# Kernel tuning notes

Measured on AMD Instinct MI355X. Metric: run time of the kernel, lower is better.

## Reference

```python
import jax, jax.numpy as jnp
import numpy as np

M, N, C = 384, 384, 16
DN = ('NCHW', 'OIHW', 'NCHW')

def _rconv(x, w):
    # real-valued 2D cross-correlation, padding=4 (9x9 kernel, SAME)
    return jax.lax.conv_general_dilated(x, w, (1, 1), ((4, 4), (4, 4)), dimension_numbers=DN)

def _cconv(x, w):
    # complex conv2d decomposed into 4 real convs (matches torch complex conv2d)
    xr, xi, wr, wi = x.real, x.imag, w.real, w.imag
    return (_rconv(xr, wr) - _rconv(xi, wi)) + 1j * (_rconv(xr, wi) + _rconv(xi, wr))

def setup_inputs() -> dict:
    key = jax.random.key(0)
    ks = jax.random.split(key, 8)
    shp = (1, M, N, 2 * C)
    kspace = jax.random.normal(ks[0], shp, jnp.float32)
    row_keep = (jax.random.uniform(ks[1], (M,)) < 0.45).astype(jnp.float32)
    kspace = kspace * row_keep[None, :, None, None]
    z = 0.1 * jax.random.normal(ks[2], shp, jnp.float32)
    prev_kspace = 0.1 * jax.random.normal(ks[3], shp, jnp.float32)
    kernel_r = 0.05 * jax.random.normal(ks[4], (1, 81, C, C), jnp.float32)
    kernel_i = 0.05 * jax.random.normal(ks[5], (1, 81, C, C), jnp.float32)
    miu = jnp.array([0.05], jnp.float32)
    spirit_kernels = jnp.zeros((1,), jnp.float32)  # unused by the module's math
    return {"z": z, "kspace": kspace, "kernel_r": kernel_r, "kernel_i": kernel_i,
            "spirit_kernels": spirit_kernels, "prev_kspace": prev_kspace, "miu": miu}

def _forward(z, kspace, kernel_r, kernel_i, prev_kspace, miu):
    divp = kspace.shape[3] // 2
    kk = kspace[0, :, :, :divp] + 1j * kspace[0, :, :, divp:]  # [m,n,C] complex64
    m, n, no_c = kk.shape
    locs = jnp.abs(kk) > 0                                     # sampling mask
    K = (kernel_r[0] + 1j * kernel_i[0]).reshape(9, 9, no_c, no_c)
    # forward SPIRiT weight: Wf[co,ci,p,q] = K[q,p,ci,co]  (torch permute (3,2,1,0))
    Wf = jnp.transpose(K, (3, 2, 1, 0))
    # adjoint weight: conj, spatial flip, swap in/out channels (exact conv_backward_new)
    Wb = jnp.transpose(jnp.conj(jnp.flip(Wf, (2, 3))), (1, 0, 2, 3))

    def G(x, W):  # [m,n,C] -> [m,n,C] via NCHW complex conv
        y = _cconv(jnp.transpose(x, (2, 0, 1))[None], W)
        return jnp.transpose(y[0], (1, 2, 0))

    mask = lambda x: jnp.where(locs, x, 0)  # selection_operator followed by its adjoint

    def ATA(x):  # x: [1,m,n,C]
        x0 = x[0]
        a2 = mask(x0)                # D^T D x
        b1 = G(x0, Wf) - x0          # (G - I) x
        b2 = G(b1, Wb) - b1          # (G - I)^H (G - I) x
        return (a2 + b2)[None]       # rho = 1

    ws = prev_kspace[:, :, :, :divp] + 1j * prev_kspace[:, :, :, divp:]
    zc = z[:, :, :, :divp] + 1j * z[:, :, :, divp:]
    am = jnp.abs(miu[0])
    DTy = mask(kk)[None]             # D^T D y (y = sampled k-space)
    p = DTy + am * zc - ATA(ws) - am * ws
    r = p
    b = ws

    def step(carry, _):
        b, p, r = carry
        q = ATA(p) + am * p
        rr = jnp.sum(r * jnp.conj(r))
        alpha = rr / jnp.sum(q * jnp.conj(p))
        b_n = b + alpha * p
        r_n = r - alpha * q
        p_n = r_n + (jnp.sum(r_n * jnp.conj(r_n)) / rr) * p
        return (b_n, p_n, r_n), None

    (b, _, _), _ = jax.lax.scan(step, (b, p, r), None, length=10)
    return jnp.concatenate([jnp.real(b), jnp.imag(b)], axis=3)

def reference(z, kspace, kernel_r, kernel_i, spirit_kernels, prev_kspace, miu):
    return _forward(z, kspace, kernel_r, kernel_i, prev_kspace, miu)
```

## Files before the change

kernel.cpp:

```cpp
#include <hip/hip_runtime.h>
#include <stdint.h>


#define MM 384
#define NPIX (MM*MM)
#define N2 (16*NPIX)
#define NRED 512
#define NCBLK 768

typedef __attribute__((ext_vector_type(8))) short short8;
typedef __attribute__((ext_vector_type(4))) float f32x4;
typedef unsigned int u32;

__device__ __forceinline__ float2 block_reduce2(float2 v) {
    #pragma unroll
    for (int off = 32; off > 0; off >>= 1) {
        v.x += __shfl_down(v.x, off);
        v.y += __shfl_down(v.y, off);
    }
    __shared__ float2 tmp[8];
    const int wid = threadIdx.x >> 6, lid = threadIdx.x & 63;
    if (lid == 0) tmp[wid] = v;
    __syncthreads();
    if (threadIdx.x == 0) {
        const int nw = blockDim.x >> 6;
        for (int i = 1; i < nw; ++i) { v.x += tmp[i].x; v.y += tmp[i].y; }
    }
    return v;
}

__device__ __forceinline__ u32 bf16rn(float f) {
    const u32 u = __float_as_uint(f);
    return (u + 0x7FFFu + ((u >> 16) & 1u)) >> 16;
}

__global__ void prep_weights(const float* __restrict__ kr, const float* __restrict__ ki,
                             u32* __restrict__ wbuf) {
    const int e = blockIdx.x * 256 + threadIdx.x;
    if (e >= 20736) return;
    const int lane = e & 63;
    int r = e >> 6;
    const int hf = r & 1; r >>= 1;
    const int q = r % 9; r /= 9;
    const int p = r % 9; r /= 9;
    const int dir = r;
    const int co = lane & 15, g = lane >> 4;
    float vv[8];
    #pragma unroll
    for (int t = 0; t < 8; ++t) {
        const int kc = 8 * g + t;
        const int ci = kc & 15;
        const int isI = kc >> 4;
        int sidx;
        if (dir == 0) sidx = (q*9 + p)*256 + ci*16 + co;
        else          sidx = ((8-q)*9 + (8-p))*256 + co*16 + ci;
        const float wr = kr[sidx];
        const float wi = (dir == 0) ? ki[sidx] : -ki[sidx];
        vv[t] = (hf == 0) ? (isI ? -wi : wr) : (isI ? wr : wi);
    }
    u32 pk[4];
    #pragma unroll
    for (int t = 0; t < 4; ++t) pk[t] = bf16rn(vv[2*t]) | (bf16rn(vv[2*t+1]) << 16);
    u32* o = wbuf + (size_t)(dir*162 + (q*9 + p)*2 + hf)*256 + lane*4;
    *(uint4*)o = make_uint4(pk[0], pk[1], pk[2], pk[3]);
}

__global__ void prep_fields(const float* __restrict__ ks, const float* __restrict__ prev,
                            float2* __restrict__ wsf, uint8_t* __restrict__ mask8) {
    const int pix = blockIdx.x * blockDim.x + threadIdx.x;
    if (pix >= NPIX) return;
    #pragma unroll
    for (int c = 0; c < 16; ++c) {
        const float krr = ks[(size_t)pix*32 + c];
        const float kii = ks[(size_t)pix*32 + c + 16];
        mask8[(size_t)c*NPIX + pix] = (krr != 0.f || kii != 0.f) ? 1 : 0;
        wsf[(size_t)c*NPIX + pix] = make_float2(prev[(size_t)pix*32 + c], prev[(size_t)pix*32 + c + 16]);
    }
}

template<int MODE>
__global__ __launch_bounds__(384, 5)
void conv9(const float2* __restrict__ x, const u32* __restrict__ Wd,
           float2* __restrict__ out, float2* __restrict__ out2,
           const float2* __restrict__ aux, const float* __restrict__ ks,
           const float* __restrict__ z, const uint8_t* __restrict__ mask8,
           const float* __restrict__ miu, float2* __restrict__ partials)
{
    __shared__ __align__(16) char Xs[20*24*64];
    __shared__ __align__(16) char Wsh[9*2048];
    const int t = threadIdx.x;
    const int bi0 = blockIdx.x;
    const int bi = (bi0 & 7) * 96 + (bi0 >> 3);
    const int i0 = (bi / 24) * 12;
    const int j0 = (bi % 24) * 16;
    const int w = t >> 6, lane = t & 63;
    const int hf = (w >= 3) ? 1 : 0;
    const int wr = w - 3*hf;
    const int m = lane & 15, g = lane >> 4;

    for (int u = t; u < 20*24; u += 384) {
        const int col = u % 24, row = u / 24;
        const int row_g = i0 - 4 + row, col_g = j0 - 4 + col;
        const bool valid = ((unsigned)row_g < MM) && ((unsigned)col_g < MM);
        const float2* src = x + (size_t)row_g*MM + col_g;
        float2 v[16];
        #pragma unroll
        for (int ci = 0; ci < 16; ++ci)
            v[ci] = valid ? src[(size_t)ci*NPIX] : make_float2(0.f, 0.f);
        u32 c0[4], c1[4], c2[4], c3[4];
        #pragma unroll
        for (int j = 0; j < 4; ++j) {
            c0[j] = bf16rn(v[2*j].x)     | (bf16rn(v[2*j+1].x) << 16);
            c1[j] = bf16rn(v[8+2*j].x)   | (bf16rn(v[9+2*j].x) << 16);
            c2[j] = bf16rn(v[2*j].y)     | (bf16rn(v[2*j+1].y) << 16);
            c3[j] = bf16rn(v[8+2*j].y)   | (bf16rn(v[9+2*j].y) << 16);
        }
        const int k3 = col & 3;
        char* pb = Xs + (size_t)(row*24 + col)*64;
        *(uint4*)(pb + (((0 ^ k3)) << 4)) = make_uint4(c0[0], c0[1], c0[2], c0[3]);
        *(uint4*)(pb + (((1 ^ k3)) << 4)) = make_uint4(c1[0], c1[1], c1[2], c1[3]);
        *(uint4*)(pb + (((2 ^ k3)) << 4)) = make_uint4(c2[0], c2[1], c2[2], c2[3]);
        *(uint4*)(pb + (((3 ^ k3)) << 4)) = make_uint4(c3[0], c3[1], c3[2], c3[3]);
    }
    __syncthreads();

    f32x4 acc[4];
    #pragma unroll
    for (int a = 0; a < 4; ++a) acc[a] = (f32x4){0.f, 0.f, 0.f, 0.f};

    const char* WdC = (const char*)Wd;
    const char* wls = Wsh + (hf << 10) + (lane << 4);

    #define MFQ(Xa, Xb, Xc, Xd, WS) do { \
        acc[0] = __builtin_amdgcn_mfma_f32_16x16x32_bf16(WS, Xa, acc[0], 0, 0, 0); \
        acc[1] = __builtin_amdgcn_mfma_f32_16x16x32_bf16(WS, Xb, acc[1], 0, 0, 0); \
        acc[2] = __builtin_amdgcn_mfma_f32_16x16x32_bf16(WS, Xc, acc[2], 0, 0, 0); \
        acc[3] = __builtin_amdgcn_mfma_f32_16x16x32_bf16(WS, Xd, acc[3], 0, 0, 0); } while (0)

    #pragma unroll 1
    for (int qq = 0; qq < 9; ++qq) {
        if (qq) __syncthreads();
        {
            const uint4* wsrc = (const uint4*)(WdC + (size_t)qq * 18432);
            uint4* wdst = (uint4*)Wsh;
            wdst[t]       = wsrc[t];
            wdst[t + 384] = wsrc[t + 384];
            wdst[t + 768] = wsrc[t + 768];
        }
        __syncthreads();

        const int colq = m + qq;
        const char* xb = Xs + (size_t)((4*wr)*24 + colq)*64 + ((g ^ (colq & 3)) << 4);
        short8 X0 = *(const short8*)(xb);
        short8 X1 = *(const short8*)(xb + 1536);
        short8 X2 = *(const short8*)(xb + 2*1536);
        short8 X3 = *(const short8*)(xb + 3*1536);
        short8 X4, WT;
        WT = *(const short8*)(wls);          X4 = *(const short8*)(xb + 4*1536);  MFQ(X0, X1, X2, X3, WT);
        WT = *(const short8*)(wls + 2048);   X0 = *(const short8*)(xb + 5*1536);  MFQ(X1, X2, X3, X4, WT);
        WT = *(const short8*)(wls + 4096);   X1 = *(const short8*)(xb + 6*1536);  MFQ(X2, X3, X4, X0, WT);
        WT = *(const short8*)(wls + 6144);   X2 = *(const short8*)(xb + 7*1536);  MFQ(X3, X4, X0, X1, WT);
        WT = *(const short8*)(wls + 8192);   X3 = *(const short8*)(xb + 8*1536);  MFQ(X4, X0, X1, X2, WT);
        WT = *(const short8*)(wls + 10240);  X4 = *(const short8*)(xb + 9*1536);  MFQ(X0, X1, X2, X3, WT);
        WT = *(const short8*)(wls + 12288);  X0 = *(const short8*)(xb + 10*1536); MFQ(X1, X2, X3, X4, WT);
        WT = *(const short8*)(wls + 14336);  X1 = *(const short8*)(xb + 11*1536); MFQ(X2, X3, X4, X0, WT);
        WT = *(const short8*)(wls + 16384);                                       MFQ(X3, X4, X0, X1, WT);
    }
    #undef MFQ

    __syncthreads();
    {
        char* base = Xs + (size_t)(((hf*12 + 4*wr)*16) + m)*64 + ((g ^ (m & 3)) << 4);
        *(f32x4*)(base)        = acc[0];
        *(f32x4*)(base + 1024) = acc[1];
        *(f32x4*)(base + 2048) = acc[2];
        *(f32x4*)(base + 3072) = acc[3];
    }
    __syncthreads();

    const float am = (MODE >= 1) ? fabsf(miu[0]) : 0.f;
    float2 part = make_float2(0.f, 0.f);
    {
        const int pair = t >> 1, ch = t & 1;
        const int co = pair & 15, row = pair >> 4;
        const int gs = co >> 2, js = co & 3;
        float re[8], im[8];
        #pragma unroll
        for (int k = 0; k < 8; ++k) {
            const int col = ch*8 + k;
            const int off = (row*16 + col)*64 + ((gs ^ (col & 3)) << 4) + js*4;
            re[k] = *(const float*)(Xs + off);
            im[k] = *(const float*)(Xs + off + 12288);
        }
        const int pixb = (i0 + row)*MM + j0 + ch*8;
        const size_t gidx = (size_t)co*NPIX + pixb;
        #pragma unroll
        for (int k = 0; k < 8; ++k) {
            if (MODE == 0) {
                const float2 tc = x[gidx + k];
                out[gidx + k] = make_float2(re[k] - tc.x, im[k] - tc.y);
            } else if (MODE == 1) {
                const float2 tc = x[gidx + k];
                const float2 pc = aux[gidx + k];
                const float mv = mask8[gidx + k] ? 1.f : 0.f;
                const float qr = re[k] - tc.x + (mv + am)*pc.x;
                const float qi = im[k] - tc.y + (mv + am)*pc.y;
                out[gidx + k] = make_float2(qr, qi);
                part.x += qr*pc.x + qi*pc.y;
                part.y += qi*pc.x - qr*pc.y;
            } else {
                const float2 tc = x[gidx + k];
                const float2 wc = aux[gidx + k];
                const float mv = mask8[gidx + k] ? 1.f : 0.f;
                const int pix = pixb + k;
                const float kcr = ks[(size_t)pix*32 + co];
                const float kci = ks[(size_t)pix*32 + co + 16];
                const float zr  = z[(size_t)pix*32 + co];
                const float zi  = z[(size_t)pix*32 + co + 16];
                const float pr = mv*kcr + am*zr - (re[k] - tc.x) - (mv + am)*wc.x;
                const float pi = mv*kci + am*zi - (im[k] - tc.y) - (mv + am)*wc.y;
                out[gidx + k]  = make_float2(pr, pi);
                out2[gidx + k] = make_float2(pr, pi);
                part.x += pr*pr + pi*pi;
            }
        }
    }
    if (MODE >= 1) {
        __syncthreads();
        part = block_reduce2(part);
        if (t == 0) partials[bi] = part;
    }
}

__global__ void finalize_rr(const float2* __restrict__ partials, float* __restrict__ scal, int n) {
    float2 s = make_float2(0.f, 0.f);
    for (int i = threadIdx.x; i < n; i += blockDim.x) { s.x += partials[i].x; s.y += partials[i].y; }
    s = block_reduce2(s);
    if (threadIdx.x == 0) scal[0] = s.x;
}

__global__ void finalize_alpha(const float2* __restrict__ partials, float* __restrict__ scal, int n) {
    float2 s = make_float2(0.f, 0.f);
    for (int i = threadIdx.x; i < n; i += blockDim.x) { s.x += partials[i].x; s.y += partials[i].y; }
    s = block_reduce2(s);
    if (threadIdx.x == 0) {
        const float rr = scal[0];
        const float d = s.x*s.x + s.y*s.y;
        scal[1] =  rr * s.x / d;
        scal[2] = -rr * s.y / d;
    }
}

__global__ void update_r(float2* __restrict__ r, const float2* __restrict__ q,
                         const float* __restrict__ scal, float2* __restrict__ partials) {
    const float ar = scal[1], ai = scal[2];
    float2 s = make_float2(0.f, 0.f);
    for (int e = blockIdx.x*256 + threadIdx.x; e < N2; e += NRED*256) {
        const float2 qv = q[e];
        float2 rv = r[e];
        rv.x -= ar*qv.x - ai*qv.y;
        rv.y -= ar*qv.y + ai*qv.x;
        r[e] = rv;
        s.x += rv.x*rv.x + rv.y*rv.y;
    }
    s = block_reduce2(s);
    if (threadIdx.x == 0) partials[blockIdx.x] = s;
}

__global__ void finalize_beta(const float2* __restrict__ partials, float* __restrict__ scal) {
    float2 v = partials[threadIdx.x];
    v = block_reduce2(v);
    if (threadIdx.x == 0) {
        const float rn = v.x;
        scal[3] = rn / scal[0];
        scal[0] = rn;
    }
}

__global__ void update_pb(float2* __restrict__ p, const float2* __restrict__ r,
                          float2* __restrict__ b, const float* __restrict__ scal) {
    const float ar = scal[1], ai = scal[2], beta = scal[3];
    const int e = blockIdx.x*256 + threadIdx.x;
    if (e < N2) {
        const float2 pv = p[e], rv = r[e];
        float2 bv = b[e];
        bv.x += ar*pv.x - ai*pv.y;
        bv.y += ar*pv.y + ai*pv.x;
        b[e] = bv;
        p[e] = make_float2(rv.x + beta*pv.x, rv.y + beta*pv.y);
    }
}

__global__ void update_bfinal(float2* __restrict__ b, const float2* __restrict__ p,
                              const float* __restrict__ scal) {
    const float ar = scal[1], ai = scal[2];
    const int e = blockIdx.x*256 + threadIdx.x;
    if (e < N2) {
        const float2 pv = p[e];
        float2 bv = b[e];
        bv.x += ar*pv.x - ai*pv.y;
        bv.y += ar*pv.y + ai*pv.x;
        b[e] = bv;
    }
}

__global__ void pack_out(const float2* __restrict__ b, float* __restrict__ out) {
    const int e = blockIdx.x*256 + threadIdx.x;
    if (e >= 32*NPIX) return;
    const int pix = e >> 5;
    const int cc  = e & 31;
    const float2 v = b[(size_t)(cc & 15)*NPIX + pix];
    out[e] = (cc < 16) ? v.x : v.y;
}

extern "C" void kernel_launch(void* const* d_in, const int* in_sizes, int n_in,
                              void* d_out, int out_size, void* d_ws, size_t ws_size,
                              hipStream_t stream) {
    const float* z    = (const float*)d_in[0];
    const float* ks   = (const float*)d_in[1];
    const float* kr   = (const float*)d_in[2];
    const float* ki   = (const float*)d_in[3];
    const float* prev = (const float*)d_in[5];
    const float* miu  = (const float*)d_in[6];
    float* out = (float*)d_out;

    char* w = (char*)d_ws;
    const size_t FB = (size_t)N2 * sizeof(float2);
    float2* wsf = (float2*)w; w += FB;
    float2* pf  = (float2*)w; w += FB;
    float2* rf  = (float2*)w; w += FB;
    float2* qf  = (float2*)w; w += FB;
    float2* tf  = (float2*)w; w += FB;
    u32* wbuf   = (u32*)w;   w += (size_t)2*162*256*sizeof(u32);
    uint8_t* mask8 = (uint8_t*)w; w += (size_t)N2;
    w = (char*)(((uintptr_t)w + 255) & ~(uintptr_t)255);
    float2* partials = (float2*)w; w += (size_t)NCBLK * sizeof(float2);
    float*  scal     = (float*)w;

    const u32* wbF = wbuf;
    const u32* wbB = wbuf + (size_t)162*256;

    prep_weights<<<81, 256, 0, stream>>>(kr, ki, wbuf);
    prep_fields<<<576, 256, 0, stream>>>(ks, prev, wsf, mask8);

    conv9<0><<<NCBLK, 384, 0, stream>>>(wsf, wbF, tf, nullptr, nullptr, nullptr, nullptr, nullptr, nullptr, nullptr);
    conv9<2><<<NCBLK, 384, 0, stream>>>(tf, wbB, pf, rf, wsf, ks, z, mask8, miu, partials);
    finalize_rr<<<1, 256, 0, stream>>>(partials, scal, NCBLK);

    for (int it = 0; it < 10; ++it) {
        conv9<0><<<NCBLK, 384, 0, stream>>>(pf, wbF, tf, nullptr, nullptr, nullptr, nullptr, nullptr, nullptr, nullptr);
        conv9<1><<<NCBLK, 384, 0, stream>>>(tf, wbB, qf, nullptr, pf, nullptr, nullptr, mask8, miu, partials);
        finalize_alpha<<<1, 256, 0, stream>>>(partials, scal, NCBLK);
        if (it < 9) {
            update_r<<<NRED, 256, 0, stream>>>(rf, qf, scal, partials);
            finalize_beta<<<1, NRED, 0, stream>>>(partials, scal);
            update_pb<<<9216, 256, 0, stream>>>(pf, rf, wsf, scal);
        } else {
            update_bfinal<<<9216, 256, 0, stream>>>(wsf, pf, scal);
        }
    }

    pack_out<<<18432, 256, 0, stream>>>(wsf, out);
}
```

Measured before the change: 1.175 ms.

## Halve conv tile height and stream weights from global instead of LDS

Cuts the conv tile from 12 to 6 output rows, doubling the block count, and shrinks the LDS input tile. Weights now go straight from global memory into registers through a three-deep rotating prefetch, removing the per-tap LDS weight staging and its barriers. Launch bounds rise to allow more resident blocks. The intent is more occupancy and fewer syncs. The cost is a larger halo overhead per block (14 rows loaded for 6 outputs) and weight reads that now depend on cache latency.

```diff
diff --git a/kernel.cpp b/kernel.cpp
--- a/kernel.cpp
+++ b/kernel.cpp
@@ -6,7 +6,7 @@
 #define NPIX (MM*MM)
 #define N2 (16*NPIX)
 #define NRED 512
-#define NCBLK 768
+#define NCBLK 1536
 
 typedef __attribute__((ext_vector_type(8))) short short8;
 typedef __attribute__((ext_vector_type(4))) float f32x4;
@@ -79,27 +79,26 @@
 }
 
 template<int MODE>
-__global__ __launch_bounds__(384, 5)
+__global__ __launch_bounds__(384, 8)
 void conv9(const float2* __restrict__ x, const u32* __restrict__ Wd,
            float2* __restrict__ out, float2* __restrict__ out2,
            const float2* __restrict__ aux, const float* __restrict__ ks,
            const float* __restrict__ z, const uint8_t* __restrict__ mask8,
            const float* __restrict__ miu, float2* __restrict__ partials)
 {
-    __shared__ __align__(16) char Xs[20*24*64];
-    __shared__ __align__(16) char Wsh[9*2048];
+    __shared__ __align__(16) char Xs[14*24*64];
     const int t = threadIdx.x;
     const int bi0 = blockIdx.x;
-    const int bi = (bi0 & 7) * 96 + (bi0 >> 3);
-    const int i0 = (bi / 24) * 12;
+    const int bi = (bi0 & 7) * 192 + (bi0 >> 3);
+    const int i0 = (bi / 24) * 6;
     const int j0 = (bi % 24) * 16;
     const int w = t >> 6, lane = t & 63;
     const int hf = (w >= 3) ? 1 : 0;
     const int wr = w - 3*hf;
     const int m = lane & 15, g = lane >> 4;
 
-    for (int u = t; u < 20*24; u += 384) {
-        const int col = u % 24, row = u / 24;
+    if (t < 14*24) {
+        const int col = t % 24, row = t / 24;
         const int row_g = i0 - 4 + row, col_g = j0 - 4 + col;
         const bool valid = ((unsigned)row_g < MM) && ((unsigned)col_g < MM);
         const float2* src = x + (size_t)row_g*MM + col_g;
@@ -124,78 +123,67 @@
     }
     __syncthreads();
 
-    f32x4 acc[4];
-    #pragma unroll
-    for (int a = 0; a < 4; ++a) acc[a] = (f32x4){0.f, 0.f, 0.f, 0.f};
-
-    const char* WdC = (const char*)Wd;
-    const char* wls = Wsh + (hf << 10) + (lane << 4);
-
-    #define MFQ(Xa, Xb, Xc, Xd, WS) do { \
+    f32x4 acc[2];
+    acc[0] = (f32x4){0.f, 0.f, 0.f, 0.f};
+    acc[1] = (f32x4){0.f, 0.f, 0.f, 0.f};
+
+    const char* wl = (const char*)Wd + (lane << 4) + (hf << 10);
+    short8 WA, WB, WC, XA, XB, XC;
+
+    #define LW(WS, TAP) do { WS = *(const short8*)(wl + (size_t)(TAP)*2048); } while (0)
+    #define MFQ2(Xa, Xb, WS) do { \
         acc[0] = __builtin_amdgcn_mfma_f32_16x16x32_bf16(WS, Xa, acc[0], 0, 0, 0); \
-        acc[1] = __builtin_amdgcn_mfma_f32_16x16x32_bf16(WS, Xb, acc[1], 0, 0, 0); \
-        acc[2] = __builtin_amdgcn_mfma_f32_16x16x32_bf16(WS, Xc, acc[2], 0, 0, 0); \
-        acc[3] = __builtin_amdgcn_mfma_f32_16x16x32_bf16(WS, Xd, acc[3], 0, 0, 0); } while (0)
+        acc[1] = __builtin_amdgcn_mfma_f32_16x16x32_bf16(WS, Xb, acc[1], 0, 0, 0); } while (0)
+
+    LW(WA, 0);  LW(WB, 1);  LW(WC, 2);
 
     #pragma unroll 1
     for (int qq = 0; qq < 9; ++qq) {
-        if (qq) __syncthreads();
-        {
-            const uint4* wsrc = (const uint4*)(WdC + (size_t)qq * 18432);
-            uint4* wdst = (uint4*)Wsh;
-            wdst[t]       = wsrc[t];
-            wdst[t + 384] = wsrc[t + 384];
-            wdst[t + 768] = wsrc[t + 768];
-        }
-        __syncthreads();
-
+        const int T0 = qq*9;
         const int colq = m + qq;
-        const char* xb = Xs + (size_t)((4*wr)*24 + colq)*64 + ((g ^ (colq & 3)) << 4);
-        short8 X0 = *(const short8*)(xb);
-        short8 X1 = *(const short8*)(xb + 1536);
-        short8 X2 = *(const short8*)(xb + 2*1536);
-        short8 X3 = *(const short8*)(xb + 3*1536);
-        short8 X4, WT;
-        WT = *(const short8*)(wls);          X4 = *(const short8*)(xb + 4*1536);  MFQ(X0, X1, X2, X3, WT);
-        WT = *(const short8*)(wls + 2048);   X0 = *(const short8*)(xb + 5*1536);  MFQ(X1, X2, X3, X4, WT);
-        WT = *(const short8*)(wls + 4096);   X1 = *(const short8*)(xb + 6*1536);  MFQ(X2, X3, X4, X0, WT);
-        WT = *(const short8*)(wls + 6144);   X2 = *(const short8*)(xb + 7*1536);  MFQ(X3, X4, X0, X1, WT);
-        WT = *(const short8*)(wls + 8192);   X3 = *(const short8*)(xb + 8*1536);  MFQ(X4, X0, X1, X2, WT);
-        WT = *(const short8*)(wls + 10240);  X4 = *(const short8*)(xb + 9*1536);  MFQ(X0, X1, X2, X3, WT);
-        WT = *(const short8*)(wls + 12288);  X0 = *(const short8*)(xb + 10*1536); MFQ(X1, X2, X3, X4, WT);
-        WT = *(const short8*)(wls + 14336);  X1 = *(const short8*)(xb + 11*1536); MFQ(X2, X3, X4, X0, WT);
-        WT = *(const short8*)(wls + 16384);                                       MFQ(X3, X4, X0, X1, WT);
-    }
-    #undef MFQ
+        const char* xb = Xs + (size_t)((2*wr)*24 + colq)*64 + ((g ^ (colq & 3)) << 4);
+        XA = *(const short8*)(xb);
+        XB = *(const short8*)(xb + 1536);
+        XC = *(const short8*)(xb + 2*1536);  MFQ2(XA, XB, WA); LW(WA, T0 + 3);
+        XA = *(const short8*)(xb + 3*1536);  MFQ2(XB, XC, WB); LW(WB, T0 + 4);
+        XB = *(const short8*)(xb + 4*1536);  MFQ2(XC, XA, WC); LW(WC, T0 + 5);
+        XC = *(const short8*)(xb + 5*1536);  MFQ2(XA, XB, WA); LW(WA, T0 + 6);
+        XA = *(const short8*)(xb + 6*1536);  MFQ2(XB, XC, WB); LW(WB, T0 + 7);
+        XB = *(const short8*)(xb + 7*1536);  MFQ2(XC, XA, WC); LW(WC, T0 + 8);
+        XC = *(const short8*)(xb + 8*1536);  MFQ2(XA, XB, WA); LW(WA, T0 + 9);
+        XA = *(const short8*)(xb + 9*1536);  MFQ2(XB, XC, WB); LW(WB, T0 + 10);
+                                             MFQ2(XC, XA, WC); LW(WC, T0 + 11);
+    }
+    #undef LW
+    #undef MFQ2
 
     __syncthreads();
     {
-        char* base = Xs + (size_t)(((hf*12 + 4*wr)*16) + m)*64 + ((g ^ (m & 3)) << 4);
+        char* base = Xs + (size_t)(((hf*6 + 2*wr)*16) + m)*64 + ((g ^ (m & 3)) << 4);
         *(f32x4*)(base)        = acc[0];
         *(f32x4*)(base + 1024) = acc[1];
-        *(f32x4*)(base + 2048) = acc[2];
-        *(f32x4*)(base + 3072) = acc[3];
     }
     __syncthreads();
 
     const float am = (MODE >= 1) ? fabsf(miu[0]) : 0.f;
     float2 part = make_float2(0.f, 0.f);
     {
-        const int pair = t >> 1, ch = t & 1;
-        const int co = pair & 15, row = pair >> 4;
+        const int row = t >> 6;
+        const int co = (t >> 2) & 15;
+        const int qt = t & 3;
         const int gs = co >> 2, js = co & 3;
-        float re[8], im[8];
+        float re[4], im[4];
         #pragma unroll
-        for (int k = 0; k < 8; ++k) {
-            const int col = ch*8 + k;
+        for (int k = 0; k < 4; ++k) {
+            const int col = qt*4 + k;
             const int off = (row*16 + col)*64 + ((gs ^ (col & 3)) << 4) + js*4;
             re[k] = *(const float*)(Xs + off);
-            im[k] = *(const float*)(Xs + off + 12288);
+            im[k] = *(const float*)(Xs + off + 6144);
         }
-        const int pixb = (i0 + row)*MM + j0 + ch*8;
+        const int pixb = (i0 + row)*MM + j0 + qt*4;
         const size_t gidx = (size_t)co*NPIX + pixb;
         #pragma unroll
-        for (int k = 0; k < 8; ++k) {
+        for (int k = 0; k < 4; ++k) {
             if (MODE == 0) {
                 const float2 tc = x[gidx + k];
                 out[gidx + k] = make_float2(re[k] - tc.x, im[k] - tc.y);
```

New measurement: 1.202 ms. +2.3%, slower.
